# Performance work log

Hardware: AMD Instinct MI355X
Metric: run time of the kernel (lower is better)

Reference implementation:

```python
import jax, jax.numpy as jnp
import numpy as np

B, S, D = 64, 2048, 512

def setup_inputs() -> dict:
    key = jax.random.key(0)
    k1, k2 = jax.random.split(key)
    features = jax.random.normal(k1, (B, S, D), dtype=jnp.float32)
    # lengths in [1, S] so every sample has at least one valid timestep
    lengths = jax.random.randint(k2, (B,), 1, S + 1, dtype=jnp.int64)
    return {"features": features, "lengths": lengths}

def reference(features, lengths):
    # mask[b, s] = s < lengths[b]
    mask = (jnp.arange(features.shape[1])[None, :] < lengths[:, None])  # [B, S]
    masked_sum = jnp.einsum('bsd,bs->bd', features, mask.astype(features.dtype))
    pooled = masked_sum / lengths.astype(features.dtype)[:, None]  # [B, D]
    return pooled
```

## Files before the change

### kernel.cpp

```cpp
#include <hip/hip_runtime.h>


#define DDIM 512
#define LD4  (DDIM / 4)
#define NS   8
#define DQ   4
#define TPB  128

__device__ __forceinline__ void acc4(float4& a, const float4& v) {
    a.x += v.x; a.y += v.y; a.z += v.z; a.w += v.w;
}

__global__ void __launch_bounds__(TPB)
pool_partial(const float* __restrict__ feat, const int* __restrict__ lengths,
             float* __restrict__ ws, int S) {
    const int b     = blockIdx.x;
    const int q     = blockIdx.y;
    const int split = blockIdx.z;
    const int t     = threadIdx.x;
    const int lane  = t & 31;
    const int rg    = t >> 5;

    const int len   = lengths[b];
    const int chunk = (len + NS - 1) / NS;
    const int s0 = split * chunk;
    if (s0 >= len) return;
    const int s1 = min(s0 + chunk, len);

    const int col = q * 32 + lane;
    const float4* __restrict__ base =
        reinterpret_cast<const float4*>(feat + (size_t)b * S * DDIM) + col;

    float4 a0 = {0.f, 0.f, 0.f, 0.f};
    float4 a1 = {0.f, 0.f, 0.f, 0.f};
    float4 a2 = {0.f, 0.f, 0.f, 0.f};
    float4 a3 = {0.f, 0.f, 0.f, 0.f};

    int s = s0 + rg;
    for (; s + 12 < s1; s += 16) {
        float4 v0 = base[(size_t)(s +  0) * LD4];
        float4 v1 = base[(size_t)(s +  4) * LD4];
        float4 v2 = base[(size_t)(s +  8) * LD4];
        float4 v3 = base[(size_t)(s + 12) * LD4];
        acc4(a0, v0); acc4(a1, v1); acc4(a2, v2); acc4(a3, v3);
    }
    for (; s < s1; s += 4) {
        float4 v = base[(size_t)s * LD4];
        acc4(a0, v);
    }
    acc4(a0, a1); acc4(a2, a3); acc4(a0, a2);

    __shared__ float4 red[TPB];
    red[t] = a0;
    __syncthreads();
    if (rg == 0) {
        acc4(a0, red[t + 32]);
        acc4(a0, red[t + 64]);
        acc4(a0, red[t + 96]);
        float4* wsp = reinterpret_cast<float4*>(ws) + ((size_t)b * NS + split) * LD4 + col;
        *wsp = a0;
    }
}

__global__ void __launch_bounds__(TPB)
pool_final(const float* __restrict__ ws, const int* __restrict__ lengths,
           float* __restrict__ out) {
    const int b    = blockIdx.x;
    const int q    = blockIdx.y;
    const int t    = threadIdx.x;
    const int lane = t & 31;
    const int rg   = t >> 5;
    const int col  = q * 32 + lane;

    const int len   = lengths[b];
    const int chunk = (len + NS - 1) / NS;
    const int nact  = (len + chunk - 1) / chunk;

    const float4* __restrict__ wsp =
        reinterpret_cast<const float4*>(ws) + (size_t)b * NS * LD4 + col;

    float4 a = {0.f, 0.f, 0.f, 0.f};
    for (int p = rg; p < nact; p += 4) {
        acc4(a, wsp[(size_t)p * LD4]);
    }

    __shared__ float4 red[TPB];
    red[t] = a;
    __syncthreads();
    if (rg == 0) {
        acc4(a, red[t + 32]);
        acc4(a, red[t + 64]);
        acc4(a, red[t + 96]);
        const float inv = 1.0f / (float)len;
        float4 r = {a.x * inv, a.y * inv, a.z * inv, a.w * inv};
        reinterpret_cast<float4*>(out + (size_t)b * DDIM)[col] = r;
    }
}

__global__ void __launch_bounds__(TPB)
pool_direct(const float* __restrict__ feat, const int* __restrict__ lengths,
            float* __restrict__ out, int S) {
    const int b   = blockIdx.x;
    const int tid = threadIdx.x;
    const int len = lengths[b];
    float4 a0 = {0.f, 0.f, 0.f, 0.f};
    float4 a1 = {0.f, 0.f, 0.f, 0.f};
    float4 a2 = {0.f, 0.f, 0.f, 0.f};
    float4 a3 = {0.f, 0.f, 0.f, 0.f};
    const float4* __restrict__ base =
        reinterpret_cast<const float4*>(feat + (size_t)b * S * DDIM) + tid;
    int s = 0;
    for (; s + 3 < len; s += 4) {
        float4 v0 = base[(size_t)(s + 0) * LD4];
        float4 v1 = base[(size_t)(s + 1) * LD4];
        float4 v2 = base[(size_t)(s + 2) * LD4];
        float4 v3 = base[(size_t)(s + 3) * LD4];
        acc4(a0, v0); acc4(a1, v1); acc4(a2, v2); acc4(a3, v3);
    }
    for (; s < len; ++s) { float4 v = base[(size_t)s * LD4]; acc4(a0, v); }
    acc4(a0, a1); acc4(a2, a3); acc4(a0, a2);
    const float inv = 1.0f / (float)len;
    float4 r = {a0.x * inv, a0.y * inv, a0.z * inv, a0.w * inv};
    reinterpret_cast<float4*>(out + (size_t)b * DDIM)[tid] = r;
}

extern "C" void kernel_launch(void* const* d_in, const int* in_sizes, int n_in,
                              void* d_out, int out_size, void* d_ws, size_t ws_size,
                              hipStream_t stream) {
    const float* feat    = (const float*)d_in[0];
    const int*   lengths = (const int*)d_in[1];
    float*       out     = (float*)d_out;

    const int B = in_sizes[1];
    const int S = in_sizes[0] / (B * DDIM);

    const size_t need = (size_t)B * NS * DDIM * sizeof(float);

    if (ws_size >= need && out_size == B * DDIM) {
        float* ws = (float*)d_ws;
        dim3 grid1(B, DQ, NS);
        dim3 grid2(B, DQ);
        pool_partial<<<grid1, TPB, 0, stream>>>(feat, lengths, ws, S);
        pool_final<<<grid2, TPB, 0, stream>>>(ws, lengths, out);
    } else {
        pool_direct<<<B, TPB, 0, stream>>>(feat, lengths, out, S);
    }
}
```

Measured before the change: 29.52 us.

## Replace fixed split grid with static-plus-atomic-queue work units of 16 rows

The partial-sum stage now splits each sample into fixed 16-row units laid out batch-minor. The first half of the units are assigned statically to blocks, and the rest are pulled from a global atomic counter, so load stays balanced across variable lengths. Each unit is handled by all 128 threads covering the full 512-wide row, replacing the per-quarter blocks and the shared-memory reduction. The cost is a memset launch, an atomic per block iteration, and a much larger partial workspace that the final kernel must read. The fast path now only runs when B=64 and S=2048.

```diff
diff --git a/kernel.cpp b/kernel.cpp
--- a/kernel.cpp
+++ b/kernel.cpp
@@ -3,62 +3,73 @@
 
 #define DDIM 512
 #define LD4  (DDIM / 4)
-#define NS   8
-#define DQ   4
 #define TPB  128
+#define RPU  16
+#define KMAX 128
+#define BMAX 64
+#define NUNITS  (BMAX * KMAX)
+#define NSTATIC 4096
+#define NQUEUED (NUNITS - NSTATIC)
+#define NBLK    (NSTATIC / 2)
 
 __device__ __forceinline__ void acc4(float4& a, const float4& v) {
     a.x += v.x; a.y += v.y; a.z += v.z; a.w += v.w;
 }
 
-__global__ void __launch_bounds__(TPB)
-pool_partial(const float* __restrict__ feat, const int* __restrict__ lengths,
-             float* __restrict__ ws, int S) {
-    const int b     = blockIdx.x;
-    const int q     = blockIdx.y;
-    const int split = blockIdx.z;
-    const int t     = threadIdx.x;
-    const int lane  = t & 31;
-    const int rg    = t >> 5;
+__device__ __forceinline__ void do_unit(unsigned u, const float4* __restrict__ featf4,
+                                        const int* __restrict__ lengths,
+                                        float4* __restrict__ wsf4, int S, int t) {
+    const int b   = (int)(u & 63u);
+    const int k   = (int)(u >> 6);
+    const int len = lengths[b];
+    const int s0  = k * RPU;
+    if (s0 >= len) return;
+    const int s1  = min(s0 + RPU, len);
 
-    const int len   = lengths[b];
-    const int chunk = (len + NS - 1) / NS;
-    const int s0 = split * chunk;
-    if (s0 >= len) return;
-    const int s1 = min(s0 + chunk, len);
+    const float4* __restrict__ base = featf4 + (size_t)b * S * LD4 + t;
 
-    const int col = q * 32 + lane;
-    const float4* __restrict__ base =
-        reinterpret_cast<const float4*>(feat + (size_t)b * S * DDIM) + col;
-
-    float4 a0 = {0.f, 0.f, 0.f, 0.f};
-    float4 a1 = {0.f, 0.f, 0.f, 0.f};
-    float4 a2 = {0.f, 0.f, 0.f, 0.f};
-    float4 a3 = {0.f, 0.f, 0.f, 0.f};
-
-    int s = s0 + rg;
-    for (; s + 12 < s1; s += 16) {
-        float4 v0 = base[(size_t)(s +  0) * LD4];
-        float4 v1 = base[(size_t)(s +  4) * LD4];
-        float4 v2 = base[(size_t)(s +  8) * LD4];
-        float4 v3 = base[(size_t)(s + 12) * LD4];
+    float4 a0 = {0.f,0.f,0.f,0.f};
+    float4 a1 = {0.f,0.f,0.f,0.f};
+    float4 a2 = {0.f,0.f,0.f,0.f};
+    float4 a3 = {0.f,0.f,0.f,0.f};
+    int s = s0;
+    for (; s + 3 < s1; s += 4) {
+        float4 v0 = base[(size_t)(s + 0) * LD4];
+        float4 v1 = base[(size_t)(s + 1) * LD4];
+        float4 v2 = base[(size_t)(s + 2) * LD4];
+        float4 v3 = base[(size_t)(s + 3) * LD4];
         acc4(a0, v0); acc4(a1, v1); acc4(a2, v2); acc4(a3, v3);
     }
-    for (; s < s1; s += 4) {
-        float4 v = base[(size_t)s * LD4];
-        acc4(a0, v);
-    }
+    for (; s < s1; ++s) acc4(a0, base[(size_t)s * LD4]);
     acc4(a0, a1); acc4(a2, a3); acc4(a0, a2);
 
-    __shared__ float4 red[TPB];
-    red[t] = a0;
-    __syncthreads();
-    if (rg == 0) {
-        acc4(a0, red[t + 32]);
-        acc4(a0, red[t + 64]);
-        acc4(a0, red[t + 96]);
-        float4* wsp = reinterpret_cast<float4*>(ws) + ((size_t)b * NS + split) * LD4 + col;
-        *wsp = a0;
+    wsf4[(size_t)u * LD4 + t] = a0;
+}
+
+__global__ void __launch_bounds__(TPB)
+pool_partial_q(const float* __restrict__ feat, const int* __restrict__ lengths,
+               float* __restrict__ ws, unsigned* __restrict__ cnt, int S) {
+    const int t = threadIdx.x;
+    const float4* featf4 = reinterpret_cast<const float4*>(feat);
+    float4* wsf4 = reinterpret_cast<float4*>(ws);
+
+    const unsigned u0 = blockIdx.x * 2u;
+    do_unit(u0,     featf4, lengths, wsf4, S, t);
+    do_unit(u0 + 1, featf4, lengths, wsf4, S, t);
+
+    __shared__ unsigned sbase;
+    for (;;) {
+        if (t == 0) {
+            sbase = __hip_atomic_fetch_add(cnt, 2u, __ATOMIC_RELAXED,
+                                           __HIP_MEMORY_SCOPE_AGENT);
+        }
+        __syncthreads();
+        const unsigned base = sbase;
+        __syncthreads();
+        if (base >= NQUEUED) break;
+        do_unit(NSTATIC + base, featf4, lengths, wsf4, S, t);
+        if (base + 1 < NQUEUED)
+            do_unit(NSTATIC + base + 1, featf4, lengths, wsf4, S, t);
     }
 }
 
@@ -72,17 +83,21 @@
     const int rg   = t >> 5;
     const int col  = q * 32 + lane;
 
-    const int len   = lengths[b];
-    const int chunk = (len + NS - 1) / NS;
-    const int nact  = (len + chunk - 1) / chunk;
+    const int len  = lengths[b];
+    const int nact = (len + RPU - 1) / RPU;
 
-    const float4* __restrict__ wsp =
-        reinterpret_cast<const float4*>(ws) + (size_t)b * NS * LD4 + col;
+    const float4* wsf4 = reinterpret_cast<const float4*>(ws);
 
-    float4 a = {0.f, 0.f, 0.f, 0.f};
-    for (int p = rg; p < nact; p += 4) {
-        acc4(a, wsp[(size_t)p * LD4]);
+    float4 a  = {0.f,0.f,0.f,0.f};
+    float4 a2 = {0.f,0.f,0.f,0.f};
+    int k = rg;
+    for (; k + 4 < nact; k += 8) {
+        float4 w0 = wsf4[(size_t)(b + 64 * k)       * LD4 + col];
+        float4 w1 = wsf4[(size_t)(b + 64 * (k + 4)) * LD4 + col];
+        acc4(a, w0); acc4(a2, w1);
     }
+    for (; k < nact; k += 4) acc4(a, wsf4[(size_t)(b + 64 * k) * LD4 + col]);
+    acc4(a, a2);
 
     __shared__ float4 red[TPB];
     red[t] = a;
@@ -103,10 +118,10 @@
     const int b   = blockIdx.x;
     const int tid = threadIdx.x;
     const int len = lengths[b];
-    float4 a0 = {0.f, 0.f, 0.f, 0.f};
-    float4 a1 = {0.f, 0.f, 0.f, 0.f};
-    float4 a2 = {0.f, 0.f, 0.f, 0.f};
-    float4 a3 = {0.f, 0.f, 0.f, 0.f};
+    float4 a0 = {0.f,0.f,0.f,0.f};
+    float4 a1 = {0.f,0.f,0.f,0.f};
+    float4 a2 = {0.f,0.f,0.f,0.f};
+    float4 a3 = {0.f,0.f,0.f,0.f};
     const float4* __restrict__ base =
         reinterpret_cast<const float4*>(feat + (size_t)b * S * DDIM) + tid;
     int s = 0;
@@ -134,13 +149,15 @@
     const int B = in_sizes[1];
     const int S = in_sizes[0] / (B * DDIM);
 
-    const size_t need = (size_t)B * NS * DDIM * sizeof(float);
+    const size_t slice_bytes = (size_t)NUNITS * DDIM * sizeof(float);
+    const size_t need = slice_bytes + sizeof(unsigned);
 
-    if (ws_size >= need && out_size == B * DDIM) {
-        float* ws = (float*)d_ws;
-        dim3 grid1(B, DQ, NS);
-        dim3 grid2(B, DQ);
-        pool_partial<<<grid1, TPB, 0, stream>>>(feat, lengths, ws, S);
+    if (B == BMAX && S == KMAX * RPU && out_size == B * DDIM && ws_size >= need) {
+        float*    ws  = (float*)d_ws;
+        unsigned* cnt = (unsigned*)((char*)d_ws + slice_bytes);
+        hipMemsetAsync(cnt, 0, sizeof(unsigned), stream);
+        dim3 grid2(B, 4);
+        pool_partial_q<<<NBLK, TPB, 0, stream>>>(feat, lengths, ws, cnt, S);
         pool_final<<<grid2, TPB, 0, stream>>>(ws, lengths, out);
     } else {
         pool_direct<<<B, TPB, 0, stream>>>(feat, lengths, out, S);
```

After: 72.16 us. 2.44x slower.
